# Kernel tuning notes

Measured on AMD Instinct MI355X. Metric: run time of the kernel, lower is better.

## Reference

```python
import jax, jax.numpy as jnp
import numpy as np
from jax import lax

IN_CH = 256
UP = 8
DN = ('NCHW', 'OIHW', 'NCHW')


def setup_inputs() -> dict:
    key = jax.random.key(0)
    ks = jax.random.split(key, 6)
    B, H, W = 8, 96, 96
    flow_lr = jax.random.normal(ks[0], (B, 2, H, W), dtype=jnp.float32)
    feat = jax.random.normal(ks[1], (B, IN_CH, H, W), dtype=jnp.float32)
    w1 = jax.random.normal(ks[2], (IN_CH, IN_CH, 3, 3), dtype=jnp.float32) * 0.02
    b1 = jnp.zeros((IN_CH,), dtype=jnp.float32)
    w2 = jax.random.normal(ks[3], (UP * UP * 9, IN_CH, 1, 1), dtype=jnp.float32) * 0.02
    b2 = jnp.zeros((UP * UP * 9,), dtype=jnp.float32)
    return {"flow_lr": flow_lr, "feat": feat, "w1": w1, "b1": b1, "w2": w2, "b2": b2}


def reference(flow_lr, feat, w1, b1, w2, b2):
    B, _, H, W = flow_lr.shape
    up = UP
    # mask head: 3x3 conv + relu + 1x1 conv
    x = lax.conv_general_dilated(feat, w1, (1, 1), 'SAME', dimension_numbers=DN)
    x = jax.nn.relu(x + b1[None, :, None, None])
    mask = lax.conv_general_dilated(x, w2, (1, 1), 'SAME', dimension_numbers=DN)
    mask = mask + b2[None, :, None, None]
    # channel dim 9*up*up splits as (9, up, up), matching torch .view(B,1,9,up,up,H,W)
    mask = mask.reshape(B, 9, up, up, H, W)
    mask = jax.nn.softmax(mask, axis=1)
    # unfold(flow_lr, 3, padding=1): 9 zero-padded 3x3 shifts, row-major (kh, kw)
    pad = jnp.pad(flow_lr, ((0, 0), (0, 0), (1, 1), (1, 1)))
    flow_unf = jnp.stack(
        [pad[:, :, i:i + H, j:j + W] for i in range(3) for j in range(3)], axis=2
    )  # (B, 2, 9, H, W)
    # convex combination over the 9 neighbors
    up_flow = jnp.einsum('bkpqhw,bckhw->bcpqhw', mask, flow_unf)  # (B,2,up,up,H,W)
    # pixel-shuffle: (B,2,p,q,H,W) -> (B,2,H,p,W,q) -> (B,2,H*up,W*up)
    up_flow = up_flow.transpose(0, 1, 4, 2, 5, 3).reshape(B, 2, H * up, W * up)
    return up_flow * up
```

## Files before the change

kernel.cpp:

```cpp
#include <hip/hip_runtime.h>
#include <hip/hip_bf16.h>
#include <stdint.h>

typedef unsigned short u16;
typedef __bf16 bf16x8 __attribute__((ext_vector_type(8)));
typedef float f32x4 __attribute__((ext_vector_type(4)));

#define MFMA16(a, b, c) __builtin_amdgcn_mfma_f32_16x16x32_bf16((a), (b), (c), 0, 0, 0)

#define GLOAD16(g, l)                                                        \
  __builtin_amdgcn_global_load_lds(                                          \
      (const __attribute__((address_space(1))) void*)(g),                    \
      (__attribute__((address_space(3))) void*)(l), 16, 0, 0)

#define SBAR() __builtin_amdgcn_s_barrier()
#define SCHEDBAR() __builtin_amdgcn_sched_barrier(0)

static __device__ __forceinline__ u16 f2bf(float f) {
  union { float f; uint32_t u; } v;
  v.f = f;
  uint32_t u = v.u;
  return (u16)((u + 0x7FFFu + ((u >> 16) & 1u)) >> 16);
}

#define FEATT_ELEMS (8u * 98u * 98u * 256u)
#define W1T_OFF     FEATT_ELEMS
#define W1T_ELEMS   (256u * 2304u)
#define W2B_OFF     (W1T_OFF + W1T_ELEMS)

__global__ __launch_bounds__(256) void halo_zero(u16* __restrict__ featT) {
  int tid = blockIdx.x * 256 + threadIdx.x;
  int b = tid / (388 * 32);
  int rem = tid % (388 * 32);
  int pos = rem >> 5, v = rem & 31;
  int h, w;
  if (pos < 98) { h = 0; w = pos; }
  else if (pos < 196) { h = 97; w = pos - 98; }
  else if (pos < 292) { h = pos - 196 + 1; w = 0; }
  else { h = pos - 292 + 1; w = 97; }
  uint4* dst = (uint4*)(featT + (size_t)((b * 98 + h) * 98 + w) * 256 + v * 8);
  *dst = make_uint4(0, 0, 0, 0);
}

__global__ __launch_bounds__(256) void prep_featT(const float* __restrict__ feat,
                                                  u16* __restrict__ featT) {
  const int pt = blockIdx.x, ct = blockIdx.y, b = blockIdx.z;
  const int p0 = pt * 64, c0 = ct * 64;
  __shared__ float tile[64][65];
  const int t = threadIdx.x;
  const int pj = t & 63, ci0 = t >> 6;
#pragma unroll
  for (int r = 0; r < 16; ++r) {
    int ci = r * 4 + ci0;
    tile[ci][pj] = feat[(b * 256 + c0 + ci) * 9216 + p0 + pj];
  }
  __syncthreads();
  const int pl = t >> 2, cc0 = (t & 3) * 16;
  const int pix = p0 + pl;
  const int h = pix / 96, w = pix % 96;
  uint32_t u[8];
#pragma unroll
  for (int i = 0; i < 8; ++i) {
    u16 lo = f2bf(tile[cc0 + 2 * i][pl]);
    u16 hi = f2bf(tile[cc0 + 2 * i + 1][pl]);
    u[i] = (uint32_t)lo | ((uint32_t)hi << 16);
  }
  uint4* dst = (uint4*)(featT + (size_t)((b * 98 + h + 1) * 98 + (w + 1)) * 256 + c0 + cc0);
  dst[0] = make_uint4(u[0], u[1], u[2], u[3]);
  dst[1] = make_uint4(u[4], u[5], u[6], u[7]);
}

__global__ __launch_bounds__(256) void prep_w(const float* __restrict__ w1,
                                              const float* __restrict__ w2,
                                              u16* __restrict__ w1t,
                                              u16* __restrict__ w2b) {
  int i = blockIdx.x * 256 + threadIdx.x;
  if (i < 589824) {
    int oc = i / 2304, r = i % 2304;
    int tap = r >> 8, cin = r & 255;
    w1t[i] = f2bf(w1[(oc * 256 + cin) * 9 + tap]);
  } else {
    int j = i - 589824;
    if (j < 147456) w2b[j] = f2bf(w2[j]);
  }
}

__global__ __launch_bounds__(512, 2) void fused(const u16* __restrict__ featT,
                                                const u16* __restrict__ w1t,
                                                const float* __restrict__ b1,
                                                const u16* __restrict__ w2b,
                                                const float* __restrict__ b2,
                                                const float* __restrict__ flow,
                                                float* __restrict__ out) {
  __shared__ __align__(16) u16 smem[61440];
  __shared__ float sFlow[2][9][96];
  __shared__ float sb1[256];
  __shared__ float sb2[576];

  const int t = threadIdx.x;
  const int wave = t >> 6, lane = t & 63;
  const int bid = blockIdx.x;
  const int mt = (bid & 7) * 96 + (bid >> 3);
  const int b = mt / 96;
  const int h0 = mt % 96;

  if (t < 256) sb1[t] = b1[t];
  for (int i = t; i < 576; i += 512) sb2[i] = b2[i];
  for (int i = t; i < 1728; i += 512) {
    int c = i / 864, rem = i % 864;
    int k = rem / 96, p = rem % 96;
    int hh = h0 + k / 3 - 1, ww = p + k % 3 - 1;
    float v = 0.f;
    if (hh >= 0 && hh < 96 && ww >= 0 && ww < 96)
      v = flow[((b * 2 + c) * 96 + hh) * 96 + ww];
    sFlow[c][k][p] = v;
  }

  const u16* aBase[2];
#pragma unroll
  for (int r = 0; r < 2; ++r) {
    int row = (r * 8 + wave) * 8 + (lane >> 3);
    int chunk = (lane & 7) ^ (row & 7);
    aBase[r] = featT + ((size_t)(b * 98 + h0 + 1) * 98 + (row + 1)) * 256 + chunk * 8;
  }
  const u16* bBase[4];
#pragma unroll
  for (int r = 0; r < 4; ++r) {
    int row = (r * 8 + wave) * 8 + (lane >> 3);
    int chunk = (lane & 7) ^ (row & 7);
    bBase[r] = w1t + (size_t)row * 2304 + chunk * 8;
  }

  auto stageA = [&](int kt, int bufi) {
    int tap = kt >> 2;
    int dh = tap / 3 - 1, dw = tap % 3 - 1;
    int aoff = (dh * 98 + dw) * 256 + (kt & 3) * 64;
    int boff = kt * 64;
    u16* base = &smem[bufi * 22528];
#pragma unroll
    for (int r = 0; r < 2; ++r) {
      int wr = r * 8 + wave;
      if (wr < 12) GLOAD16(aBase[r] + aoff, base + wr * 512);
    }
#pragma unroll
    for (int r = 0; r < 4; ++r)
      GLOAD16(bBase[r] + boff, base + 6144 + (r * 8 + wave) * 512);
  };

  const int wm = wave >> 2, wn = wave & 3;
  int aoffs[3][2], boffs[4][2];
#pragma unroll
  for (int ki = 0; ki < 2; ++ki) {
    int kc = ki * 4 + (lane >> 4);
#pragma unroll
    for (int m = 0; m < 3; ++m) {
      int rowa = wm * 48 + m * 16 + (lane & 15);
      aoffs[m][ki] = rowa * 64 + ((kc ^ (rowa & 7)) * 8);
    }
#pragma unroll
    for (int n = 0; n < 4; ++n) {
      int rowb = wn * 64 + n * 16 + (lane & 15);
      boffs[n][ki] = rowb * 64 + ((kc ^ (rowb & 7)) * 8);
    }
  }

  f32x4 acc[3][4];
#pragma unroll
  for (int m = 0; m < 3; ++m)
#pragma unroll
    for (int n = 0; n < 4; ++n) acc[m][n] = f32x4{0.f, 0.f, 0.f, 0.f};

  auto computeA = [&](int bufi) {
    const u16* base = &smem[bufi * 22528];
    __builtin_amdgcn_s_setprio(1);
#pragma unroll
    for (int ki = 0; ki < 2; ++ki) {
      bf16x8 av[3], bv[4];
#pragma unroll
      for (int m = 0; m < 3; ++m) av[m] = *(const bf16x8*)&base[aoffs[m][ki]];
#pragma unroll
      for (int n = 0; n < 4; ++n) bv[n] = *(const bf16x8*)&base[6144 + boffs[n][ki]];
#pragma unroll
      for (int m = 0; m < 3; ++m)
#pragma unroll
        for (int n = 0; n < 4; ++n) acc[m][n] = MFMA16(av[m], bv[n], acc[m][n]);
    }
    __builtin_amdgcn_s_setprio(0);
  };

  __syncthreads();
  stageA(0, 0);
  stageA(1, 1);

  for (int kt = 0; kt < 34; ++kt) {
    asm volatile("s_waitcnt vmcnt(5)" ::: "memory");
    SBAR();
    SCHEDBAR();
    computeA(kt & 1);
    asm volatile("s_waitcnt lgkmcnt(0)" ::: "memory");
    SBAR();
    SCHEDBAR();
    stageA(kt + 2, kt & 1);
  }
  asm volatile("s_waitcnt vmcnt(5)" ::: "memory");
  SBAR(); SCHEDBAR();
  computeA(0);
  asm volatile("s_waitcnt lgkmcnt(0)" ::: "memory");
  SBAR(); SCHEDBAR();
  asm volatile("s_waitcnt vmcnt(0)" ::: "memory");
  SBAR(); SCHEDBAR();
  computeA(1);
  __syncthreads();

  const int g4 = (lane >> 4) << 2;
#pragma unroll
  for (int m = 0; m < 3; ++m) {
    int pixr = wm * 48 + m * 16 + g4;
#pragma unroll
    for (int n = 0; n < 4; ++n) {
      int oc = wn * 64 + n * 16 + (lane & 15);
      float bias = sb1[oc];
      f32x4 v = acc[m][n];
#pragma unroll
      for (int j = 0; j < 4; ++j) {
        int pix = pixr + j;
        float val = v[j] + bias;
        val = val > 0.f ? val : 0.f;
        smem[pix * 256 + (((oc >> 3) ^ (pix & 7)) * 8) + (oc & 7)] = f2bf(val);
      }
    }
  }
  __syncthreads();

  auto stageB = [&](int step, int bufi) {
    int cI = step >> 1, kh = step & 1;
    u16* base = &smem[24576 + bufi * 18432];
#pragma unroll
    for (int r = 0; r < 5; ++r) {
      int wr = r * 8 + wave;
      if (wr < 36) {
        int row = wr * 4 + (lane >> 4);
        int chan = (row >> 4) * 64 + cI * 16 + (row & 15);
        int c = lane & 15;
        const u16* src = w2b + (size_t)chan * 256 + kh * 128 + ((c ^ (row & 15)) * 8);
        GLOAD16(src, base + wr * 512);
      }
    }
  };

  stageB(0, 0);
  stageB(1, 1);
  bf16x8 areg[8];
  const int pixl = wave * 16 + (lane & 15);
  if (wave < 6) {
#pragma unroll
    for (int s = 0; s < 8; ++s) {
      int kc = s * 4 + (lane >> 4);
      areg[s] = *(const bf16x8*)&smem[pixl * 256 + ((kc ^ (pixl & 7)) * 8)];
    }
  }

  f32x4 acc2[9];
#pragma unroll
  for (int step = 0; step < 8; ++step) {
    if (step == 7) asm volatile("s_waitcnt vmcnt(0)" ::: "memory");
    else           asm volatile("s_waitcnt vmcnt(4)" ::: "memory");
    SBAR();
    SCHEDBAR();
    const int kh = step & 1, cI = step >> 1;
    const int bufc = step & 1;
    if (wave < 6) {
      if (kh == 0) {
#pragma unroll
        for (int nf = 0; nf < 9; ++nf) acc2[nf] = f32x4{0.f, 0.f, 0.f, 0.f};
      }
      const u16* base = &smem[24576 + bufc * 18432];
      __builtin_amdgcn_s_setprio(1);
#pragma unroll
      for (int ki = 0; ki < 4; ++ki) {
        bf16x8 a = areg[kh * 4 + ki];
        int kc = ki * 4 + (lane >> 4);
#pragma unroll
        for (int nf = 0; nf < 9; ++nf) {
          int row = nf * 16 + (lane & 15);
          bf16x8 bv = *(const bf16x8*)&base[row * 128 + ((kc ^ (row & 15)) * 8)];
          acc2[nf] = MFMA16(a, bv, acc2[nf]);
        }
      }
      __builtin_amdgcn_s_setprio(0);
      if (kh == 1) {
        int pql = lane & 15;
        int p = cI * 2 + (pql >> 3), q = pql & 7;
#pragma unroll
        for (int j = 0; j < 4; ++j) {
          int pe = wave * 16 + g4 + j;
          float v[9], mx = -3.0e38f;
#pragma unroll
          for (int nf = 0; nf < 9; ++nf) {
            v[nf] = acc2[nf][j] + sb2[nf * 64 + cI * 16 + pql];
            mx = fmaxf(mx, v[nf]);
          }
          float s = 0.f, fx = 0.f, fy = 0.f;
#pragma unroll
          for (int nf = 0; nf < 9; ++nf) {
            float e = __expf(v[nf] - mx);
            s += e;
            fx += e * sFlow[0][nf][pe];
            fy += e * sFlow[1][nf][pe];
          }
          float sc = 8.0f / s;
          size_t o0 = ((size_t)(b * 2 + 0) * 768 + h0 * 8 + p) * 768 + pe * 8 + q;
          size_t o1 = ((size_t)(b * 2 + 1) * 768 + h0 * 8 + p) * 768 + pe * 8 + q;
          out[o0] = fx * sc;
          out[o1] = fy * sc;
        }
      }
    }
    asm volatile("s_waitcnt lgkmcnt(0)" ::: "memory");
    SBAR();
    SCHEDBAR();
    if (step < 6) stageB(step + 2, step & 1);
  }
}

extern "C" void kernel_launch(void* const* d_in, const int* in_sizes, int n_in,
                              void* d_out, int out_size, void* d_ws, size_t ws_size,
                              hipStream_t stream) {
  const float* flow = (const float*)d_in[0];
  const float* feat = (const float*)d_in[1];
  const float* w1 = (const float*)d_in[2];
  const float* b1 = (const float*)d_in[3];
  const float* w2 = (const float*)d_in[4];
  const float* b2 = (const float*)d_in[5];
  float* out = (float*)d_out;
  u16* ws = (u16*)d_ws;
  u16* featT = ws;
  u16* w1t = ws + W1T_OFF;
  u16* w2b = ws + W2B_OFF;

  halo_zero<<<388, 256, 0, stream>>>(featT);
  prep_featT<<<dim3(144, 4, 8), 256, 0, stream>>>(feat, featT);
  prep_w<<<2880, 256, 0, stream>>>(w1, w2, w1t, w2b);
  fused<<<768, 512, 0, stream>>>(featT, w1t, b1, w2b, b2, flow, out);
}
```

Baseline: 205.8 us.

## Shrink fused conv tile to 64 pixels with 256 threads for higher occupancy

Restructures the fused mask-head kernel from 96-pixel row tiles with 512 threads to 64-pixel flat tiles with 256 threads, giving 1152 blocks and a target of three blocks per CU. The K step drops to 32 so LDS per block shrinks, and the 1x1 conv stage loads smaller w2 chunks over more pipeline steps. Flow neighbors are kept in LDS as bf16, and biases are now read from global memory instead of shared. The aim is better occupancy and load balance across CUs. The cost is twice as many barrier-separated K iterations, less MFMA work per LDS load, and a small precision loss on the flow values.

```diff
diff --git a/kernel.cpp b/kernel.cpp
--- a/kernel.cpp
+++ b/kernel.cpp
@@ -15,12 +15,19 @@
 
 #define SBAR() __builtin_amdgcn_s_barrier()
 #define SCHEDBAR() __builtin_amdgcn_sched_barrier(0)
+#define VMCNT(n) asm volatile("s_waitcnt vmcnt(" #n ")" ::: "memory")
+#define LGKM0() asm volatile("s_waitcnt lgkmcnt(0)" ::: "memory")
 
 static __device__ __forceinline__ u16 f2bf(float f) {
   union { float f; uint32_t u; } v;
   v.f = f;
   uint32_t u = v.u;
   return (u16)((u + 0x7FFFu + ((u >> 16) & 1u)) >> 16);
+}
+static __device__ __forceinline__ float bf2f(u16 u) {
+  union { uint32_t u; float f; } v;
+  v.u = ((uint32_t)u) << 16;
+  return v.f;
 }
 
 #define FEATT_ELEMS (8u * 98u * 98u * 256u)
@@ -85,106 +92,93 @@
   }
 }
 
-__global__ __launch_bounds__(512, 2) void fused(const u16* __restrict__ featT,
+__global__ __launch_bounds__(256, 3) void fused(const u16* __restrict__ featT,
                                                 const u16* __restrict__ w1t,
-                                                const float* __restrict__ b1,
+                                                const float* __restrict__ b1g,
                                                 const u16* __restrict__ w2b,
-                                                const float* __restrict__ b2,
+                                                const float* __restrict__ b2g,
                                                 const float* __restrict__ flow,
                                                 float* __restrict__ out) {
-  __shared__ __align__(16) u16 smem[61440];
-  __shared__ float sFlow[2][9][96];
-  __shared__ float sb1[256];
-  __shared__ float sb2[576];
+  __shared__ __align__(16) u16 smem[26752];
 
   const int t = threadIdx.x;
   const int wave = t >> 6, lane = t & 63;
   const int bid = blockIdx.x;
-  const int mt = (bid & 7) * 96 + (bid >> 3);
-  const int b = mt / 96;
-  const int h0 = mt % 96;
-
-  if (t < 256) sb1[t] = b1[t];
-  for (int i = t; i < 576; i += 512) sb2[i] = b2[i];
-  for (int i = t; i < 1728; i += 512) {
-    int c = i / 864, rem = i % 864;
-    int k = rem / 96, p = rem % 96;
-    int hh = h0 + k / 3 - 1, ww = p + k % 3 - 1;
+  const int mt = (bid & 7) * 144 + (bid >> 3);
+  const int b = mt / 144;
+  const int ipl0 = (mt % 144) * 64;
+
+  for (int i = t; i < 1152; i += 256) {
+    int c = i / 576, rem = i % 576;
+    int k = rem >> 6, p = rem & 63;
+    int ip = ipl0 + p;
+    int h = ip / 96, w = ip % 96;
+    int hh = h + k / 3 - 1, ww = w + k % 3 - 1;
     float v = 0.f;
     if (hh >= 0 && hh < 96 && ww >= 0 && ww < 96)
       v = flow[((b * 2 + c) * 96 + hh) * 96 + ww];
-    sFlow[c][k][p] = v;
-  }
-
-  const u16* aBase[2];
-#pragma unroll
-  for (int r = 0; r < 2; ++r) {
-    int row = (r * 8 + wave) * 8 + (lane >> 3);
-    int chunk = (lane & 7) ^ (row & 7);
-    aBase[r] = featT + ((size_t)(b * 98 + h0 + 1) * 98 + (row + 1)) * 256 + chunk * 8;
-  }
-  const u16* bBase[4];
-#pragma unroll
-  for (int r = 0; r < 4; ++r) {
-    int row = (r * 8 + wave) * 8 + (lane >> 3);
-    int chunk = (lane & 7) ^ (row & 7);
-    bBase[r] = w1t + (size_t)row * 2304 + chunk * 8;
+    smem[25600 + i] = f2bf(v);
+  }
+
+  const int pA = wave * 16 + (lane >> 2);
+  const u16* aSrc;
+  {
+    int ip = ipl0 + pA;
+    int h = ip / 96, w = ip % 96;
+    int cs = (lane & 3) ^ ((pA >> 1) & 3);
+    aSrc = featT + ((size_t)(b * 98 + h + 1) * 98 + (w + 1)) * 256 + cs * 8;
+  }
+  const u16* bSrc[4];
+#pragma unroll
+  for (int i = 0; i < 4; ++i) {
+    int oc = (i * 4 + wave) * 16 + (lane >> 2);
+    int cs = (lane & 3) ^ ((oc >> 1) & 3);
+    bSrc[i] = w1t + (size_t)oc * 2304 + cs * 8;
   }
 
   auto stageA = [&](int kt, int bufi) {
-    int tap = kt >> 2;
+    int tap = kt >> 3;
     int dh = tap / 3 - 1, dw = tap % 3 - 1;
-    int aoff = (dh * 98 + dw) * 256 + (kt & 3) * 64;
-    int boff = kt * 64;
-    u16* base = &smem[bufi * 22528];
-#pragma unroll
-    for (int r = 0; r < 2; ++r) {
-      int wr = r * 8 + wave;
-      if (wr < 12) GLOAD16(aBase[r] + aoff, base + wr * 512);
-    }
+    int aoff = (dh * 98 + dw) * 256 + (kt & 7) * 32;
+    int boff = kt * 32;
+    u16* db = &smem[bufi * 10240];
+    GLOAD16(aSrc + aoff, db + wave * 512);
 #pragma unroll
     for (int r = 0; r < 4; ++r)
-      GLOAD16(bBase[r] + boff, base + 6144 + (r * 8 + wave) * 512);
+      GLOAD16(bSrc[r] + boff, db + 2048 + (r * 4 + wave) * 512);
   };
 
-  const int wm = wave >> 2, wn = wave & 3;
-  int aoffs[3][2], boffs[4][2];
-#pragma unroll
-  for (int ki = 0; ki < 2; ++ki) {
-    int kc = ki * 4 + (lane >> 4);
-#pragma unroll
-    for (int m = 0; m < 3; ++m) {
-      int rowa = wm * 48 + m * 16 + (lane & 15);
-      aoffs[m][ki] = rowa * 64 + ((kc ^ (rowa & 7)) * 8);
-    }
-#pragma unroll
-    for (int n = 0; n < 4; ++n) {
-      int rowb = wn * 64 + n * 16 + (lane & 15);
-      boffs[n][ki] = rowb * 64 + ((kc ^ (rowb & 7)) * 8);
-    }
-  }
-
-  f32x4 acc[3][4];
-#pragma unroll
-  for (int m = 0; m < 3; ++m)
+  f32x4 acc[4][4];
+#pragma unroll
+  for (int m = 0; m < 4; ++m)
 #pragma unroll
     for (int n = 0; n < 4; ++n) acc[m][n] = f32x4{0.f, 0.f, 0.f, 0.f};
 
+  const int l15 = lane & 15, kc = lane >> 4;
+  int aoffs[4], boffs[4];
+#pragma unroll
+  for (int m = 0; m < 4; ++m) {
+    int r = m * 16 + l15;
+    aoffs[m] = r * 32 + ((kc ^ ((r >> 1) & 3)) * 8);
+  }
+#pragma unroll
+  for (int n = 0; n < 4; ++n) {
+    int oc = wave * 64 + n * 16 + l15;
+    boffs[n] = (64 + oc) * 32 + ((kc ^ ((oc >> 1) & 3)) * 8);
+  }
+
   auto computeA = [&](int bufi) {
-    const u16* base = &smem[bufi * 22528];
+    const u16* base = &smem[bufi * 10240];
     __builtin_amdgcn_s_setprio(1);
-#pragma unroll
-    for (int ki = 0; ki < 2; ++ki) {
-      bf16x8 av[3], bv[4];
-#pragma unroll
-      for (int m = 0; m < 3; ++m) av[m] = *(const bf16x8*)&base[aoffs[m][ki]];
-#pragma unroll
-      for (int n = 0; n < 4; ++n) bv[n] = *(const bf16x8*)&base[6144 + boffs[n][ki]];
-#pragma unroll
-      for (int m = 0; m < 3; ++m)
-#pragma unroll
-        for (int n = 0; n < 4; ++n) acc[m][n] = MFMA16(av[m], bv[n], acc[m][n]);
-    }
+    bf16x8 av[4], bv[4];
+#pragma unroll
+    for (int m = 0; m < 4; ++m) av[m] = *(const bf16x8*)&base[aoffs[m]];
+#pragma unroll
+    for (int n = 0; n < 4; ++n) bv[n] = *(const bf16x8*)&base[boffs[n]];
+#pragma unroll
+    for (int m = 0; m < 4; ++m)
+#pragma unroll
+      for (int n = 0; n < 4; ++n) acc[m][n] = MFMA16(av[m], bv[n], acc[m][n]);
     __builtin_amdgcn_s_setprio(0);
   };
 
@@ -192,34 +186,29 @@
   stageA(0, 0);
   stageA(1, 1);
 
-  for (int kt = 0; kt < 34; ++kt) {
-    asm volatile("s_waitcnt vmcnt(5)" ::: "memory");
-    SBAR();
-    SCHEDBAR();
+  for (int kt = 0; kt < 70; ++kt) {
+    VMCNT(5);
+    SBAR(); SCHEDBAR();
     computeA(kt & 1);
-    asm volatile("s_waitcnt lgkmcnt(0)" ::: "memory");
-    SBAR();
-    SCHEDBAR();
+    LGKM0();
+    SBAR(); SCHEDBAR();
     stageA(kt + 2, kt & 1);
   }
-  asm volatile("s_waitcnt vmcnt(5)" ::: "memory");
-  SBAR(); SCHEDBAR();
+  VMCNT(5); SBAR(); SCHEDBAR();
   computeA(0);
-  asm volatile("s_waitcnt lgkmcnt(0)" ::: "memory");
-  SBAR(); SCHEDBAR();
-  asm volatile("s_waitcnt vmcnt(0)" ::: "memory");
-  SBAR(); SCHEDBAR();
+  LGKM0(); SBAR(); SCHEDBAR();
+  VMCNT(0); SBAR(); SCHEDBAR();
   computeA(1);
   __syncthreads();
 
-  const int g4 = (lane >> 4) << 2;
-#pragma unroll
-  for (int m = 0; m < 3; ++m) {
-    int pixr = wm * 48 + m * 16 + g4;
+  const int g4 = kc << 2;
+#pragma unroll
+  for (int m = 0; m < 4; ++m) {
+    int pixr = m * 16 + g4;
 #pragma unroll
     for (int n = 0; n < 4; ++n) {
-      int oc = wn * 64 + n * 16 + (lane & 15);
-      float bias = sb1[oc];
+      int oc = wave * 64 + n * 16 + l15;
+      float bias = b1g[oc];
       f32x4 v = acc[m][n];
 #pragma unroll
       for (int j = 0; j < 4; ++j) {
@@ -232,64 +221,53 @@
   }
   __syncthreads();
 
-  auto stageB = [&](int step, int bufi) {
-    int cI = step >> 1, kh = step & 1;
-    u16* base = &smem[24576 + bufi * 18432];
-#pragma unroll
-    for (int r = 0; r < 5; ++r) {
-      int wr = r * 8 + wave;
-      if (wr < 36) {
-        int row = wr * 4 + (lane >> 4);
-        int chan = (row >> 4) * 64 + cI * 16 + (row & 15);
-        int c = lane & 15;
-        const u16* src = w2b + (size_t)chan * 256 + kh * 128 + ((c ^ (row & 15)) * 8);
-        GLOAD16(src, base + wr * 512);
+  auto stageC = [&](int cI, int k8, int bufi) {
+    u16* db = &smem[16384 + bufi * 4608];
+#pragma unroll
+    for (int i = 0; i < 3; ++i) {
+      int g = i * 4 + wave;
+      if (g < 9) {
+        int n = g * 16 + (lane >> 2);
+        int chan = (n >> 4) * 64 + cI * 16 + (n & 15);
+        int cs = (lane & 3) ^ ((n >> 1) & 3);
+        GLOAD16(w2b + (size_t)chan * 256 + k8 * 32 + cs * 8, db + g * 512);
       }
     }
   };
 
-  stageB(0, 0);
-  stageB(1, 1);
+  stageC(0, 0, 0);
+  stageC(0, 1, 1);
+
   bf16x8 areg[8];
-  const int pixl = wave * 16 + (lane & 15);
-  if (wave < 6) {
-#pragma unroll
-    for (int s = 0; s < 8; ++s) {
-      int kc = s * 4 + (lane >> 4);
-      areg[s] = *(const bf16x8*)&smem[pixl * 256 + ((kc ^ (pixl & 7)) * 8)];
-    }
+  const int pixl = wave * 16 + l15;
+#pragma unroll
+  for (int s = 0; s < 8; ++s) {
+    int kco = s * 4 + kc;
+    areg[s] = *(const bf16x8*)&smem[pixl * 256 + ((kco ^ (pixl & 7)) * 8)];
   }
 
   f32x4 acc2[9];
-#pragma unroll
-  for (int step = 0; step < 8; ++step) {
-    if (step == 7) asm volatile("s_waitcnt vmcnt(0)" ::: "memory");
-    else           asm volatile("s_waitcnt vmcnt(4)" ::: "memory");
-    SBAR();
-    SCHEDBAR();
-    const int kh = step & 1, cI = step >> 1;
-    const int bufc = step & 1;
-    if (wave < 6) {
-      if (kh == 0) {
+  for (int cI = 0; cI < 4; ++cI) {
+#pragma unroll
+    for (int k8 = 0; k8 < 8; ++k8) {
+      if (cI == 3 && k8 == 7) { VMCNT(0); } else { VMCNT(2); }
+      SBAR(); SCHEDBAR();
+      if (k8 == 0) {
 #pragma unroll
         for (int nf = 0; nf < 9; ++nf) acc2[nf] = f32x4{0.f, 0.f, 0.f, 0.f};
       }
-      const u16* base = &smem[24576 + bufc * 18432];
+      const u16* base = &smem[16384 + (k8 & 1) * 4608];
+      bf16x8 a = areg[k8];
       __builtin_amdgcn_s_setprio(1);
 #pragma unroll
-      for (int ki = 0; ki < 4; ++ki) {
-        bf16x8 a = areg[kh * 4 + ki];
-        int kc = ki * 4 + (lane >> 4);
-#pragma unroll
-        for (int nf = 0; nf < 9; ++nf) {
-          int row = nf * 16 + (lane & 15);
-          bf16x8 bv = *(const bf16x8*)&base[row * 128 + ((kc ^ (row & 15)) * 8)];
-          acc2[nf] = MFMA16(a, bv, acc2[nf]);
-        }
+      for (int nf = 0; nf < 9; ++nf) {
+        int n = nf * 16 + l15;
+        bf16x8 bv = *(const bf16x8*)&base[n * 32 + ((kc ^ ((n >> 1) & 3)) * 8)];
+        acc2[nf] = MFMA16(a, bv, acc2[nf]);
       }
       __builtin_amdgcn_s_setprio(0);
-      if (kh == 1) {
-        int pql = lane & 15;
+      if (k8 == 7) {
+        int pql = l15;
         int p = cI * 2 + (pql >> 3), q = pql & 7;
 #pragma unroll
         for (int j = 0; j < 4; ++j) {
@@ -297,7 +275,7 @@
           float v[9], mx = -3.0e38f;
 #pragma unroll
           for (int nf = 0; nf < 9; ++nf) {
-            v[nf] = acc2[nf][j] + sb2[nf * 64 + cI * 16 + pql];
+            v[nf] = acc2[nf][j] + b2g[nf * 64 + cI * 16 + pql];
             mx = fmaxf(mx, v[nf]);
           }
           float s = 0.f, fx = 0.f, fy = 0.f;
@@ -305,21 +283,22 @@
           for (int nf = 0; nf < 9; ++nf) {
             float e = __expf(v[nf] - mx);
             s += e;
-            fx += e * sFlow[0][nf][pe];
-            fy += e * sFlow[1][nf][pe];
+            fx += e * bf2f(smem[25600 + nf * 64 + pe]);
+            fy += e * bf2f(smem[25600 + 576 + nf * 64 + pe]);
           }
           float sc = 8.0f / s;
-          size_t o0 = ((size_t)(b * 2 + 0) * 768 + h0 * 8 + p) * 768 + pe * 8 + q;
-          size_t o1 = ((size_t)(b * 2 + 1) * 768 + h0 * 8 + p) * 768 + pe * 8 + q;
+          int ip = ipl0 + pe;
+          int h = ip / 96, w = ip % 96;
+          size_t o0 = ((size_t)(b * 2 + 0) * 768 + h * 8 + p) * 768 + w * 8 + q;
+          size_t o1 = ((size_t)(b * 2 + 1) * 768 + h * 8 + p) * 768 + w * 8 + q;
           out[o0] = fx * sc;
           out[o1] = fy * sc;
         }
       }
+      LGKM0();
+      SBAR(); SCHEDBAR();
+      if (!(cI == 3 && k8 >= 6)) stageC(cI + (k8 >= 6 ? 1 : 0), (k8 + 2) & 7, k8 & 1);
     }
-    asm volatile("s_waitcnt lgkmcnt(0)" ::: "memory");
-    SBAR();
-    SCHEDBAR();
-    if (step < 6) stageB(step + 2, step & 1);
   }
 }
 
@@ -341,5 +320,5 @@
   halo_zero<<<388, 256, 0, stream>>>(featT);
   prep_featT<<<dim3(144, 4, 8), 256, 0, stream>>>(feat, featT);
   prep_w<<<2880, 256, 0, stream>>>(w1, w2, w1t, w2b);
-  fused<<<768, 512, 0, stream>>>(featT, w1t, b1, w2b, b2, flow, out);
-}
+  fused<<<1152, 256, 0, stream>>>(featT, w1t, b1, w2b, b2, flow, out);
+}
```

After: 194.5 us. 5.5% less time.
